# Optimization experiments

Hardware: AMD Instinct MI355X
Metric: run time of the kernel (lower is better)

## Reference

```python
import jax, jax.numpy as jnp
import numpy as np

EPS = 1e-5  # torch LayerNorm default

def ln(x, g, b):
    mu = jnp.mean(x, axis=-1, keepdims=True)
    var = jnp.mean((x - mu) ** 2, axis=-1, keepdims=True)
    return (x - mu) * jax.lax.rsqrt(var + EPS) * g + b

B, S, E, A = 131072, 199, 3, 32
D_IN = S + 1  # state_dim + 1 (time feature)

def setup_inputs() -> dict:
    key = jax.random.key(0)
    ks = iter(jax.random.split(key, 32))
    def w(shape, fan_in):
        lim = 1.0 / np.sqrt(fan_in)
        return jax.random.uniform(next(ks), shape, jnp.float32, -lim, lim)
    inp = {
        "state": jax.random.normal(next(ks), (B, S), jnp.float32),
        "time_delta": jax.random.uniform(next(ks), (B,), jnp.float32),
        # trunk: Linear(200,256)+LN, Linear(256,256)+LN, Linear(256,128)+LN
        "W1": w((D_IN, 256), D_IN), "b1": w((256,), D_IN),
        "g1": jnp.ones((256,), jnp.float32), "be1": jnp.zeros((256,), jnp.float32),
        "W2": w((256, 256), 256), "b2": w((256,), 256),
        "g2": jnp.ones((256,), jnp.float32), "be2": jnp.zeros((256,), jnp.float32),
        "W3": w((256, 128), 256), "b3": w((128,), 256),
        "g3": jnp.ones((128,), jnp.float32), "be3": jnp.zeros((128,), jnp.float32),
        # value stream
        "Wv1": w((128, 64), 128), "bv1": w((64,), 128),
        "gv": jnp.ones((64,), jnp.float32), "bev": jnp.zeros((64,), jnp.float32),
        "Wv2": w((64, 1), 64), "bv2": w((1,), 64),
        # E stacked advantage streams (all heads share action dim A)
        "Wa1": w((E, 128, 64), 128), "ba1": w((E, 64), 128),
        "ga": jnp.ones((E, 64), jnp.float32), "bea": jnp.zeros((E, 64), jnp.float32),
        "Wa2": w((E, 64, A), 64), "ba2": w((E, A), 64),
        "event_type": jax.random.randint(next(ks), (B,), 0, E),
    }
    return inp

def reference(state, time_delta,
              W1, b1, g1, be1, W2, b2, g2, be2, W3, b3, g3, be3,
              Wv1, bv1, gv, bev, Wv2, bv2,
              Wa1, ba1, ga, bea, Wa2, ba2, event_type):
    td = time_delta[:, None]                       # [B,1]
    x = jnp.concatenate([state, td], axis=1)       # [B,200]
    h = jax.nn.relu(ln(x @ W1 + b1, g1, be1))      # [B,256]
    h = jax.nn.relu(ln(h @ W2 + b2, g2, be2))      # [B,256]
    f = jax.nn.relu(ln(h @ W3 + b3, g3, be3))      # [B,128]
    v = jax.nn.relu(ln(f @ Wv1 + bv1, gv, bev)) @ Wv2 + bv2  # [B,1]
    # compute all E advantage heads, then per-sample select by event_type
    h1 = jnp.einsum('bd,edh->ebh', f, Wa1) + ba1[:, None, :]           # [E,B,64]
    h1 = jax.nn.relu(ln(h1, ga[:, None, :], bea[:, None, :]))
    adv_all = jnp.einsum('ebh,eha->eba', h1, Wa2) + ba2[:, None, :]    # [E,B,A]
    adv = jnp.take_along_axis(adv_all, event_type[None, :, None], axis=0)[0]  # [B,A]
    return v + (adv - adv.mean(axis=1, keepdims=True))
```

## Files before the change

### kernel.cpp

```cpp
#include <hip/hip_runtime.h>
#include <hip/hip_bf16.h>
#include <stdint.h>

#define DEV __device__ __forceinline__

typedef __attribute__((ext_vector_type(8))) short short8;
typedef __attribute__((ext_vector_type(4))) float floatx4;

constexpr int TM  = 64;
constexpr int NB  = 131072;
constexpr int AST = 264;

constexpr int OFF_W1 = 0;
constexpr int OFF_W2 = 57344;
constexpr int OFF_W3 = 122880;
constexpr int OFF_WH = 155648;
constexpr int OFF_WA2= 188416;
constexpr int NWQ    = 194560;

constexpr int C_B1=0, C_G1=256, C_BE1=512, C_B2=768, C_G2=1024, C_BE2=1280,
  C_B3=1536, C_G3=1664, C_BE3=1792, C_BV1=1920, C_GV=1984, C_BEV=2048,
  C_WV2=2112, C_BV2=2176, C_BA1=2177, C_GA=2369, C_BEA=2561, C_BA2=2753;
constexpr int NCONST=2849;

struct Ptrs {
  const float *state,*td,*W1,*b1,*g1,*be1,*W2,*b2,*g2,*be2,*W3,*b3,*g3,*be3,
    *Wv1,*bv1,*gv,*bev,*Wv2,*bv2,*Wa1,*ba1,*ga,*bea,*Wa2,*ba2;
  const int *et;
};

DEV unsigned short f2bf(float x){
  uint32_t u = __float_as_uint(x);
  u += 0x7fffu + ((u>>16)&1u);
  return (unsigned short)(u>>16);
}
DEV uint32_t f2bf_pk(float a, float b){
  float2 f2; f2.x=a; f2.y=b;
  __hip_bfloat162 h = __float22bfloat162_rn(f2);
  union { __hip_bfloat162 h; uint32_t u; } cv; cv.h = h;
  return cv.u;
}

__global__ void prep_kernel(Ptrs p, unsigned short* __restrict__ wq, float* __restrict__ cq){
  int idx = blockIdx.x*256 + threadIdx.x;
  if (idx < NWQ) {
    float v = 0.f;
    if (idx < OFF_W2) {
      int e = idx, w = e/14336, r = e%14336;
      int kc = r>>11, ct=(r>>9)&3, l=(r>>3)&63, j=r&7;
      int n = w*64 + ct*16 + (l&15);
      int k = kc*32 + (l>>4)*8 + j;
      if (k < 200) v = p.W1[k*256 + n];
      else if (k == 200) v = p.b1[n];
    } else if (idx < OFF_W3) {
      int e = idx-OFF_W2, w=e>>14, r=e&16383;
      int kc=r>>11, ct=(r>>9)&3, l=(r>>3)&63, j=r&7;
      int n = w*64 + ct*16 + (l&15);
      int k = kc*32 + (l>>4)*8 + j;
      int c = (k & ~63) + 16*(k&3) + ((k&63)>>2);
      v = p.W2[c*256 + n];
    } else if (idx < OFF_WH) {
      int e = idx-OFF_W3, w=e>>13, r=e&8191;
      int kc=r>>10, ct=(r>>9)&1, l=(r>>3)&63, j=r&7;
      int n = w*32 + ct*16 + (l&15);
      int k = kc*32 + (l>>4)*8 + j;
      int c = (k & ~63) + 16*(k&3) + ((k&63)>>2);
      v = p.W3[c*128 + n];
    } else if (idx < OFF_WA2) {
      int e = idx-OFF_WH, h=e>>13, r=e&8191;
      int kc=r>>11, ct=(r>>9)&3, l=(r>>3)&63, j=r&7;
      int n = ct*16 + (l&15);
      int k = kc*32 + (l>>4)*8 + j;
      int c = (k & ~31) + 16*(k&1) + ((k&31)>>1);
      v = (h<3) ? p.Wa1[h*8192 + c*64 + n] : p.Wv1[c*64 + n];
    } else {
      int e = idx-OFF_WA2, h=e>>11, r=e&2047;
      int kc=r>>10, ct=(r>>9)&1, l=(r>>3)&63, j=r&7;
      int n = ct*16 + (l&15);
      int k = kc*32 + (l>>4)*8 + j;
      int c = 16*(k&3) + (k>>2);
      v = p.Wa2[h*2048 + c*32 + n];
    }
    wq[idx] = f2bf(v);
  } else if (idx < NWQ + NCONST) {
    int ci = idx - NWQ;
    const float* src; int off;
    if      (ci < 256)  { src=p.b1;  off=ci; }
    else if (ci < 512)  { src=p.g1;  off=ci-256; }
    else if (ci < 768)  { src=p.be1; off=ci-512; }
    else if (ci < 1024) { src=p.b2;  off=ci-768; }
    else if (ci < 1280) { src=p.g2;  off=ci-1024; }
    else if (ci < 1536) { src=p.be2; off=ci-1280; }
    else if (ci < 1664) { src=p.b3;  off=ci-1536; }
    else if (ci < 1792) { src=p.g3;  off=ci-1664; }
    else if (ci < 1920) { src=p.be3; off=ci-1792; }
    else if (ci < 1984) { src=p.bv1; off=ci-1920; }
    else if (ci < 2048) { src=p.gv;  off=ci-1984; }
    else if (ci < 2112) { src=p.bev; off=ci-2048; }
    else if (ci < 2176) { src=p.Wv2; off=ci-2112; }
    else if (ci < 2177) { src=p.bv2; off=ci-2176; }
    else if (ci < 2369) { src=p.ba1; off=ci-2177; }
    else if (ci < 2561) { src=p.ga;  off=ci-2369; }
    else if (ci < 2753) { src=p.bea; off=ci-2561; }
    else                { src=p.ba2; off=ci-2753; }
    cq[ci] = src[off];
  }
}

template<int N>
DEV void loadB(short8 (&B)[N], const unsigned short* __restrict__ src, int lane){
  #pragma unroll
  for (int i=0;i<N;i++) B[i] = *(const short8*)(src + i*512 + lane*8);
}

template<int CT>
DEV void zeroAcc(floatx4 (&acc)[4][4]){
  const floatx4 z = {0.f,0.f,0.f,0.f};
  #pragma unroll
  for (int rt=0;rt<4;rt++)
    #pragma unroll
    for (int ct=0;ct<CT;ct++) acc[rt][ct]=z;
}

template<int KC,int CT>
DEV void runGemm(floatx4 (&acc)[4][4], const short8 (&B)[KC*CT],
                 const unsigned short* aBase, int aOff){
  #pragma unroll
  for (int kc=0;kc<KC;kc++){
    short8 a[4];
    #pragma unroll
    for (int rt=0;rt<4;rt++)
      a[rt] = *(const short8*)(aBase + rt*16*AST + aOff + kc*32);
    #pragma unroll
    for (int rt=0;rt<4;rt++)
      #pragma unroll
      for (int ct=0;ct<CT;ct++)
        acc[rt][ct] = __builtin_amdgcn_mfma_f32_16x16x32_bf16(a[rt], B[kc*CT+ct], acc[rt][ct], 0,0,0);
  }
}

template<int CT,bool BIAS>
DEV void statsAtomic(const floatx4 (&acc)[4][4], const float* __restrict__ cq, int bo, int colBase,
                     float* sbuf, float* ssbuf, int ln, int q, float (&bias)[4]){
  #pragma unroll
  for (int ct=0;ct<CT;ct++) bias[ct] = BIAS ? cq[bo+colBase+ct*16+ln] : 0.f;
  #pragma unroll
  for (int rt=0;rt<4;rt++){
    float s[4]={0,0,0,0}, ss[4]={0,0,0,0};
    #pragma unroll
    for (int ct=0;ct<CT;ct++){
      #pragma unroll
      for (int r=0;r<4;r++){
        float v=acc[rt][ct][r]+bias[ct];
        s[r]+=v; ss[r]+=v*v;
      }
    }
    #pragma unroll
    for (int r=0;r<4;r++){
      #pragma unroll
      for (int d=1;d<16;d<<=1){ s[r]+=__shfl_xor(s[r],d); ss[r]+=__shfl_xor(ss[r],d); }
      if (ln==0){
        int row = rt*16+q*4+r;
        atomicAdd(&sbuf[row],  s[r]);
        atomicAdd(&ssbuf[row], ss[r]);
      }
    }
  }
}

template<int CT>
DEV void lnWrite(const floatx4 (&acc)[4][4], const float* __restrict__ cq, int go, int beo, int colBase,
                 const float* sbuf, const float* ssbuf, float invN,
                 unsigned short* act_, int ln, int q, const float (&bias)[4]){
  float g[CT], be[CT];
  #pragma unroll
  for (int ct=0;ct<CT;ct++){ g[ct]=cq[go+colBase+ct*16+ln]; be[ct]=cq[beo+colBase+ct*16+ln]; }
  #pragma unroll
  for (int rt=0;rt<4;rt++){
    floatx4 sv  = *(const floatx4*)&sbuf [rt*16+q*4];
    floatx4 ssv = *(const floatx4*)&ssbuf[rt*16+q*4];
    #pragma unroll
    for (int r=0;r<4;r++){
      float mu = sv[r]*invN;
      float rs = rsqrtf(ssv[r]*invN - mu*mu + 1e-5f);
      int row=rt*16+q*4+r;
      unsigned short* pp = act_ + row*AST + colBase + ln*CT;
      float y[CT];
      #pragma unroll
      for (int ct=0;ct<CT;ct++)
        y[ct] = fmaxf((acc[rt][ct][r]+bias[ct]-mu)*rs*g[ct]+be[ct], 0.f);
      if constexpr (CT==4){
        uint2 pk; pk.x = f2bf_pk(y[0],y[1]); pk.y = f2bf_pk(y[2],y[3]);
        *(uint2*)pp = pk;
      } else {
        *(uint32_t*)pp = f2bf_pk(y[0],y[1]);
      }
    }
  }
}

__global__ __launch_bounds__(256,4) void dqn_main(
    const float* __restrict__ state, const float* __restrict__ td,
    const int* __restrict__ et, const unsigned short* __restrict__ wq,
    const float* __restrict__ cq, float* __restrict__ out)
{
  __shared__ __align__(16) unsigned short act[TM*AST];
  __shared__ float sstat[2][2][64];
  __shared__ float vbuf[64];
  __shared__ int   etl[64];

  const int tid=threadIdx.x, w=tid>>6, lane=tid&63, q=lane>>4, ln=lane&15;
  const int rowBlk = blockIdx.x*TM;

  {
    ((float*)sstat)[tid] = 0.f;
    const float* sbase = state + (size_t)rowBlk*199;
    for (int i=tid; i<64*199; i+=256){
      float v = sbase[i];
      int row = i/199, col = i - row*199;
      act[row*AST+col] = f2bf(v);
    }
    for (int i=tid; i<64*32; i+=256){
      int row = i>>5, c = 199 + (i&31);
      unsigned short hv = 0;
      if (c==199) hv = f2bf(td[rowBlk+row]);
      else if (c==200) hv = 0x3F80u;
      act[row*AST+c] = hv;
    }
    if (tid < 64) etl[tid] = et[rowBlk+tid];
  }
  __syncthreads();

  const unsigned short* aBase = act + ln*AST + q*8;
  floatx4 acc[4][4];
  float bias[4];

  {
    short8 B[28];
    loadB<28>(B, wq + OFF_W1 + w*14336, lane);
    zeroAcc<4>(acc);
    runGemm<7,4>(acc, B, aBase, 0);
  }
  statsAtomic<4,false>(acc, cq, 0, w*64, sstat[0][0], sstat[0][1], ln, q, bias);
  __syncthreads();
  lnWrite<4>(acc, cq, C_G1, C_BE1, w*64, sstat[0][0], sstat[0][1], 1.f/256.f, act, ln, q, bias);
  __syncthreads();

  {
    short8 B[32];
    loadB<32>(B, wq + OFF_W2 + w*16384, lane);
    zeroAcc<4>(acc);
    runGemm<8,4>(acc, B, aBase, 0);
  }
  statsAtomic<4,true>(acc, cq, C_B2, w*64, sstat[1][0], sstat[1][1], ln, q, bias);
  __syncthreads();
  if (tid < 128) ((float*)sstat[0])[tid] = 0.f;
  lnWrite<4>(acc, cq, C_G2, C_BE2, w*64, sstat[1][0], sstat[1][1], 1.f/256.f, act, ln, q, bias);
  __syncthreads();

  {
    short8 B[16];
    loadB<16>(B, wq + OFF_W3 + w*8192, lane);
    zeroAcc<2>(acc);
    runGemm<8,2>(acc, B, aBase, 0);
  }
  statsAtomic<2,true>(acc, cq, C_B3, w*32, sstat[0][0], sstat[0][1], ln, q, bias);
  __syncthreads();
  lnWrite<2>(acc, cq, C_G3, C_BE3, w*32, sstat[0][0], sstat[0][1], 1.f/128.f, act, ln, q, bias);
  __syncthreads();

  {
    short8 B[16];
    loadB<16>(B, wq + OFF_WH + w*8192, lane);
    zeroAcc<4>(acc);
    runGemm<4,4>(acc, B, aBase, 0);
  }
  {
    const int bo = (w<3)? C_BA1+w*64 : C_BV1;
    const int go = (w<3)? C_GA +w*64 : C_GV;
    const int beo= (w<3)? C_BEA+w*64 : C_BEV;
    float bi[4], g[4], be[4];
    #pragma unroll
    for (int ct=0;ct<4;ct++){ bi[ct]=cq[bo+ct*16+ln]; g[ct]=cq[go+ct*16+ln]; be[ct]=cq[beo+ct*16+ln]; }
    float wv[4]; float bv2v = 0.f;
    if (w==3){
      #pragma unroll
      for (int ct=0;ct<4;ct++) wv[ct]=cq[C_WV2+ct*16+ln];
      bv2v = cq[C_BV2];
    }
    #pragma unroll
    for (int rt=0;rt<4;rt++){
      float y[4][4];
      float s[4]={0,0,0,0}, ss[4]={0,0,0,0};
      #pragma unroll
      for (int ct=0;ct<4;ct++)
        #pragma unroll
        for (int r=0;r<4;r++){
          float v=acc[rt][ct][r]+bi[ct];
          y[ct][r]=v; s[r]+=v; ss[r]+=v*v;
        }
      #pragma unroll
      for (int r=0;r<4;r++){
        #pragma unroll
        for (int d=1;d<16;d<<=1){ s[r]+=__shfl_xor(s[r],d); ss[r]+=__shfl_xor(ss[r],d); }
        float mu=s[r]*(1.f/64.f);
        float rs=rsqrtf(ss[r]*(1.f/64.f)-mu*mu+1e-5f);
        #pragma unroll
        for (int ct=0;ct<4;ct++)
          y[ct][r]=fmaxf((y[ct][r]-mu)*rs*g[ct]+be[ct], 0.f);
      }

      if (w==3){
        float dd[4]={0,0,0,0};
        #pragma unroll
        for (int ct=0;ct<4;ct++)
          #pragma unroll
          for (int r=0;r<4;r++) dd[r]+=y[ct][r]*wv[ct];
        #pragma unroll
        for (int r=0;r<4;r++){
          #pragma unroll
          for (int d=1;d<16;d<<=1) dd[r]+=__shfl_xor(dd[r],d);
          if (ln==0) vbuf[rt*16+q*4+r]=dd[r]+bv2v;
        }
      } else {
        #pragma unroll
        for (int r=0;r<4;r++){
          int row=rt*16+q*4+r;
          (void)row;
        }
      }
      if (w<3){
        #pragma unroll
        for (int ct=0;ct<4;ct++)
          #pragma unroll
          for (int r=0;r<4;r++) acc[rt][ct][r]=y[ct][r];
      }
    }
  }
  __syncthreads();

  if (w<3){
    #pragma unroll
    for (int rt=0;rt<4;rt++)
      #pragma unroll
      for (int r=0;r<4;r++){
        int row=rt*16+q*4+r;
        unsigned short* pp = act + row*AST + 64*w + ln*4;
        uint2 pk;
        pk.x = f2bf_pk(acc[rt][0][r], acc[rt][1][r]);
        pk.y = f2bf_pk(acc[rt][2][r], acc[rt][3][r]);
        *(uint2*)pp = pk;
      }
    short8 B2[4];
    loadB<4>(B2, wq + OFF_WA2 + w*2048, lane);
    zeroAcc<2>(acc);
    runGemm<2,2>(acc, B2, aBase, 64*w);
    float b20 = cq[C_BA2 + w*32 + ln];
    float b21 = cq[C_BA2 + w*32 + 16 + ln];
    #pragma unroll
    for (int rt=0;rt<4;rt++)
      #pragma unroll
      for (int r=0;r<4;r++){
        float a0 = acc[rt][0][r] + b20;
        float a1 = acc[rt][1][r] + b21;
        float sm = a0 + a1;
        #pragma unroll
        for (int d=1;d<16;d<<=1) sm += __shfl_xor(sm,d);
        int row = rt*16+q*4+r;
        if (etl[row]==w){
          float vv = vbuf[row];
          float m  = sm*(1.f/32.f);
          float* op = out + (size_t)(rowBlk+row)*32 + ln;
          op[0]  = vv + a0 - m;
          op[16] = vv + a1 - m;
        }
      }
  }
}

extern "C" void kernel_launch(void* const* d_in, const int* in_sizes, int n_in,
                              void* d_out, int out_size, void* d_ws, size_t ws_size,
                              hipStream_t stream)
{
  Ptrs p;
  p.state=(const float*)d_in[0];  p.td =(const float*)d_in[1];
  p.W1 =(const float*)d_in[2];  p.b1 =(const float*)d_in[3];  p.g1 =(const float*)d_in[4];  p.be1=(const float*)d_in[5];
  p.W2 =(const float*)d_in[6];  p.b2 =(const float*)d_in[7];  p.g2 =(const float*)d_in[8];  p.be2=(const float*)d_in[9];
  p.W3 =(const float*)d_in[10]; p.b3 =(const float*)d_in[11]; p.g3 =(const float*)d_in[12]; p.be3=(const float*)d_in[13];
  p.Wv1=(const float*)d_in[14]; p.bv1=(const float*)d_in[15]; p.gv =(const float*)d_in[16]; p.bev=(const float*)d_in[17];
  p.Wv2=(const float*)d_in[18]; p.bv2=(const float*)d_in[19];
  p.Wa1=(const float*)d_in[20]; p.ba1=(const float*)d_in[21]; p.ga =(const float*)d_in[22]; p.bea=(const float*)d_in[23];
  p.Wa2=(const float*)d_in[24]; p.ba2=(const float*)d_in[25];
  p.et =(const int*)d_in[26];

  unsigned short* wq = (unsigned short*)d_ws;
  float* cq = (float*)((char*)d_ws + (size_t)NWQ*2);

  const int prepN = NWQ + NCONST;
  hipLaunchKernelGGL(prep_kernel, dim3((prepN+255)/256), dim3(256), 0, stream, p, wq, cq);
  hipLaunchKernelGGL(dqn_main, dim3(NB/TM), dim3(256), 0, stream,
                     p.state, p.td, p.et, (const unsigned short*)wq, (const float*)cq, (float*)d_out);
}
```

Baseline: 310.2 us.

## Use 128-row tiles with 512 threads and row-owned head layers per wave

```diff
diff --git a/kernel.cpp b/kernel.cpp
--- a/kernel.cpp
+++ b/kernel.cpp
@@ -7,7 +7,7 @@
 typedef __attribute__((ext_vector_type(8))) short short8;
 typedef __attribute__((ext_vector_type(4))) float floatx4;
 
-constexpr int TM  = 64;
+constexpr int TM  = 128;
 constexpr int NB  = 131072;
 constexpr int AST = 264;
 
@@ -71,7 +71,7 @@
       int kc=r>>11, ct=(r>>9)&3, l=(r>>3)&63, j=r&7;
       int n = ct*16 + (l&15);
       int k = kc*32 + (l>>4)*8 + j;
-      int c = (k & ~31) + 16*(k&1) + ((k&31)>>1);
+      int c = 16*(k&7) + (k>>3);
       v = (h<3) ? p.Wa1[h*8192 + c*64 + n] : p.Wv1[c*64 + n];
     } else {
       int e = idx-OFF_WA2, h=e>>11, r=e&2047;
@@ -107,48 +107,45 @@
   }
 }
 
-template<int N>
-DEV void loadB(short8 (&B)[N], const unsigned short* __restrict__ src, int lane){
-  #pragma unroll
-  for (int i=0;i<N;i++) B[i] = *(const short8*)(src + i*512 + lane*8);
-}
-
-template<int CT>
-DEV void zeroAcc(floatx4 (&acc)[4][4]){
+DEV void zeroAcc44(floatx4 (&acc)[4][4]){
   const floatx4 z = {0.f,0.f,0.f,0.f};
   #pragma unroll
   for (int rt=0;rt<4;rt++)
     #pragma unroll
-    for (int ct=0;ct<CT;ct++) acc[rt][ct]=z;
-}
-
-template<int KC,int CT>
-DEV void runGemm(floatx4 (&acc)[4][4], const short8 (&B)[KC*CT],
-                 const unsigned short* aBase, int aOff){
+    for (int ct=0;ct<4;ct++) acc[rt][ct]=z;
+}
+
+template<int KC>
+DEV void runGemm44(floatx4 (&acc)[4][4], const unsigned short* __restrict__ wsrc,
+                   const unsigned short* aBase, int lane){
   #pragma unroll
   for (int kc=0;kc<KC;kc++){
+    short8 b[4];
+    #pragma unroll
+    for (int ct=0;ct<4;ct++)
+      b[ct] = *(const short8*)(wsrc + kc*2048 + ct*512 + lane*8);
     short8 a[4];
     #pragma unroll
     for (int rt=0;rt<4;rt++)
-      a[rt] = *(const short8*)(aBase + rt*16*AST + aOff + kc*32);
+      a[rt] = *(const short8*)(aBase + rt*16*AST + kc*32);
     #pragma unroll
     for (int rt=0;rt<4;rt++)
       #pragma unroll
-      for (int ct=0;ct<CT;ct++)
-        acc[rt][ct] = __builtin_amdgcn_mfma_f32_16x16x32_bf16(a[rt], B[kc*CT+ct], acc[rt][ct], 0,0,0);
-  }
-}
-
-template<int CT,bool BIAS>
+      for (int ct=0;ct<4;ct++)
+        acc[rt][ct] = __builtin_amdgcn_mfma_f32_16x16x32_bf16(a[rt], b[ct], acc[rt][ct], 0,0,0);
+  }
+}
+
+template<bool BIAS>
 DEV void statsAtomic(const floatx4 (&acc)[4][4], const float* __restrict__ cq, int bo, int colBase,
-                     float* sbuf, float* ssbuf, int ln, int q, float (&bias)[4]){
-  #pragma unroll
-  for (int ct=0;ct<CT;ct++) bias[ct] = BIAS ? cq[bo+colBase+ct*16+ln] : 0.f;
+                     int rowBase, float* sbuf, float* ssbuf, int ln, int q, float (&bias)[4]){
+  #pragma unroll
+  for (int ct=0;ct<4;ct++) bias[ct] = BIAS ? cq[bo+colBase+ct*16+ln] : 0.f;
   #pragma unroll
   for (int rt=0;rt<4;rt++){
     float s[4]={0,0,0,0}, ss[4]={0,0,0,0};
     #pragma unroll
-    for (int ct=0;ct<CT;ct++){
+    for (int ct=0;ct<4;ct++){
       #pragma unroll
       for (int r=0;r<4;r++){
         float v=acc[rt][ct][r]+bias[ct];
@@ -160,7 +157,7 @@
       #pragma unroll
       for (int d=1;d<16;d<<=1){ s[r]+=__shfl_xor(s[r],d); ss[r]+=__shfl_xor(ss[r],d); }
       if (ln==0){
-        int row = rt*16+q*4+r;
+        int row = rowBase + rt*16+q*4+r;
         atomicAdd(&sbuf[row],  s[r]);
         atomicAdd(&ssbuf[row], ss[r]);
       }
@@ -168,213 +165,216 @@
   }
 }
 
-template<int CT>
-DEV void lnWrite(const floatx4 (&acc)[4][4], const float* __restrict__ cq, int go, int beo, int colBase,
-                 const float* sbuf, const float* ssbuf, float invN,
-                 unsigned short* act_, int ln, int q, const float (&bias)[4]){
-  float g[CT], be[CT];
-  #pragma unroll
-  for (int ct=0;ct<CT;ct++){ g[ct]=cq[go+colBase+ct*16+ln]; be[ct]=cq[beo+colBase+ct*16+ln]; }
+DEV void lnWrite44(const floatx4 (&acc)[4][4], const float* __restrict__ cq, int go, int beo,
+                   int colBase, int rowBase, const float* sbuf, const float* ssbuf, float invN,
+                   unsigned short* act_, int ln, int q, const float (&bias)[4]){
+  float g[4], be[4];
+  #pragma unroll
+  for (int ct=0;ct<4;ct++){ g[ct]=cq[go+colBase+ct*16+ln]; be[ct]=cq[beo+colBase+ct*16+ln]; }
   #pragma unroll
   for (int rt=0;rt<4;rt++){
-    floatx4 sv  = *(const floatx4*)&sbuf [rt*16+q*4];
-    floatx4 ssv = *(const floatx4*)&ssbuf[rt*16+q*4];
+    floatx4 sv  = *(const floatx4*)&sbuf [rowBase + rt*16+q*4];
+    floatx4 ssv = *(const floatx4*)&ssbuf[rowBase + rt*16+q*4];
     #pragma unroll
     for (int r=0;r<4;r++){
       float mu = sv[r]*invN;
       float rs = rsqrtf(ssv[r]*invN - mu*mu + 1e-5f);
-      int row=rt*16+q*4+r;
-      unsigned short* pp = act_ + row*AST + colBase + ln*CT;
-      float y[CT];
-      #pragma unroll
-      for (int ct=0;ct<CT;ct++)
+      int row = rowBase + rt*16+q*4+r;
+      float y[4];
+      #pragma unroll
+      for (int ct=0;ct<4;ct++)
         y[ct] = fmaxf((acc[rt][ct][r]+bias[ct]-mu)*rs*g[ct]+be[ct], 0.f);
-      if constexpr (CT==4){
-        uint2 pk; pk.x = f2bf_pk(y[0],y[1]); pk.y = f2bf_pk(y[2],y[3]);
-        *(uint2*)pp = pk;
-      } else {
-        *(uint32_t*)pp = f2bf_pk(y[0],y[1]);
-      }
-    }
-  }
-}
-
-__global__ __launch_bounds__(256,4) void dqn_main(
+      uint2 pk; pk.x = f2bf_pk(y[0],y[1]); pk.y = f2bf_pk(y[2],y[3]);
+      *(uint2*)(act_ + row*AST + colBase + ln*4) = pk;
+    }
+  }
+}
+
+__global__ __launch_bounds__(512,2) void dqn_main(
     const float* __restrict__ state, const float* __restrict__ td,
     const int* __restrict__ et, const unsigned short* __restrict__ wq,
     const float* __restrict__ cq, float* __restrict__ out)
 {
   __shared__ __align__(16) unsigned short act[TM*AST];
-  __shared__ float sstat[2][2][64];
-  __shared__ float vbuf[64];
-  __shared__ int   etl[64];
+  __shared__ float sstat[2][2][TM];
 
   const int tid=threadIdx.x, w=tid>>6, lane=tid&63, q=lane>>4, ln=lane&15;
+  const int wr=w>>2, wc=w&3;
   const int rowBlk = blockIdx.x*TM;
 
   {
     ((float*)sstat)[tid] = 0.f;
-    const float* sbase = state + (size_t)rowBlk*199;
-    for (int i=tid; i<64*199; i+=256){
-      float v = sbase[i];
-      int row = i/199, col = i - row*199;
-      act[row*AST+col] = f2bf(v);
-    }
-    for (int i=tid; i<64*32; i+=256){
-      int row = i>>5, c = 199 + (i&31);
-      unsigned short hv = 0;
-      if (c==199) hv = f2bf(td[rowBlk+row]);
-      else if (c==200) hv = 0x3F80u;
-      act[row*AST+c] = hv;
-    }
-    if (tid < 64) etl[tid] = et[rowBlk+tid];
+    const int row = tid>>2, t = tid&3;
+    const float* srow = state + (size_t)(rowBlk+row)*199;
+    unsigned short* arow = act + row*AST;
+    #pragma unroll
+    for (int jj=0; jj<25; jj++){
+      int c = (t*25+jj)*2;
+      float v0 = srow[c];
+      float v1 = (c==198) ? td[rowBlk+row] : srow[c+1];
+      *(uint32_t*)(arow + c) = f2bf_pk(v0, v1);
+    }
+    if (t==0) *(uint32_t*)(arow + 200) = 0x00003F80u;
+    #pragma unroll
+    for (int z=0; z<3; z++)
+      *(uint32_t*)(arow + 202 + t*6 + z*2) = 0u;
   }
   __syncthreads();
 
-  const unsigned short* aBase = act + ln*AST + q*8;
   floatx4 acc[4][4];
   float bias[4];
+  const unsigned short* aBase12 = act + (wr*64 + ln)*AST + q*8;
+
+  zeroAcc44(acc);
+  runGemm44<7>(acc, wq + OFF_W1 + wc*14336, aBase12, lane);
+  statsAtomic<false>(acc, cq, 0, wc*64, wr*64, sstat[0][0], sstat[0][1], ln, q, bias);
+  __syncthreads();
+  lnWrite44(acc, cq, C_G1, C_BE1, wc*64, wr*64, sstat[0][0], sstat[0][1], 1.f/256.f, act, ln, q, bias);
+  __syncthreads();
+
+  zeroAcc44(acc);
+  runGemm44<8>(acc, wq + OFF_W2 + wc*16384, aBase12, lane);
+  statsAtomic<true>(acc, cq, C_B2, wc*64, wr*64, sstat[1][0], sstat[1][1], ln, q, bias);
+  __syncthreads();
+  lnWrite44(acc, cq, C_G2, C_BE2, wc*64, wr*64, sstat[1][0], sstat[1][1], 1.f/256.f, act, ln, q, bias);
+  __syncthreads();
+
+  const unsigned short* aR = act + (16*w + ln)*AST + q*8;
+  int etv[4];
+  #pragma unroll
+  for (int r=0;r<4;r++) etv[r] = et[rowBlk + 16*w + q*4 + r];
 
   {
-    short8 B[28];
-    loadB<28>(B, wq + OFF_W1 + w*14336, lane);
-    zeroAcc<4>(acc);
-    runGemm<7,4>(acc, B, aBase, 0);
-  }
-  statsAtomic<4,false>(acc, cq, 0, w*64, sstat[0][0], sstat[0][1], ln, q, bias);
-  __syncthreads();
-  lnWrite<4>(acc, cq, C_G1, C_BE1, w*64, sstat[0][0], sstat[0][1], 1.f/256.f, act, ln, q, bias);
-  __syncthreads();
-
-  {
-    short8 B[32];
-    loadB<32>(B, wq + OFF_W2 + w*16384, lane);
-    zeroAcc<4>(acc);
-    runGemm<8,4>(acc, B, aBase, 0);
-  }
-  statsAtomic<4,true>(acc, cq, C_B2, w*64, sstat[1][0], sstat[1][1], ln, q, bias);
-  __syncthreads();
-  if (tid < 128) ((float*)sstat[0])[tid] = 0.f;
-  lnWrite<4>(acc, cq, C_G2, C_BE2, w*64, sstat[1][0], sstat[1][1], 1.f/256.f, act, ln, q, bias);
-  __syncthreads();
-
-  {
-    short8 B[16];
-    loadB<16>(B, wq + OFF_W3 + w*8192, lane);
-    zeroAcc<2>(acc);
-    runGemm<8,2>(acc, B, aBase, 0);
-  }
-  statsAtomic<2,true>(acc, cq, C_B3, w*32, sstat[0][0], sstat[0][1], ln, q, bias);
-  __syncthreads();
-  lnWrite<2>(acc, cq, C_G3, C_BE3, w*32, sstat[0][0], sstat[0][1], 1.f/128.f, act, ln, q, bias);
-  __syncthreads();
-
-  {
-    short8 B[16];
-    loadB<16>(B, wq + OFF_WH + w*8192, lane);
-    zeroAcc<4>(acc);
-    runGemm<4,4>(acc, B, aBase, 0);
-  }
-  {
-    const int bo = (w<3)? C_BA1+w*64 : C_BV1;
-    const int go = (w<3)? C_GA +w*64 : C_GV;
-    const int beo= (w<3)? C_BEA+w*64 : C_BEV;
+    floatx4 a8[8];
+    const floatx4 z = {0.f,0.f,0.f,0.f};
+    #pragma unroll
+    for (int nt=0;nt<8;nt++) a8[nt]=z;
+    #pragma unroll
+    for (int kc=0;kc<8;kc++){
+      short8 a = *(const short8*)(aR + kc*32);
+      #pragma unroll
+      for (int nt=0;nt<8;nt++){
+        short8 b = *(const short8*)(wq + OFF_W3 + (nt>>1)*8192 + kc*1024 + (nt&1)*512 + lane*8);
+        a8[nt] = __builtin_amdgcn_mfma_f32_16x16x32_bf16(a, b, a8[nt], 0,0,0);
+      }
+    }
+    float bi[8], g[8], be[8];
+    #pragma unroll
+    for (int nt=0;nt<8;nt++){
+      bi[nt]=cq[C_B3+nt*16+ln]; g[nt]=cq[C_G3+nt*16+ln]; be[nt]=cq[C_BE3+nt*16+ln];
+    }
+    #pragma unroll
+    for (int r=0;r<4;r++){
+      float s=0, ss=0;
+      #pragma unroll
+      for (int nt=0;nt<8;nt++){ float v=a8[nt][r]+bi[nt]; s+=v; ss+=v*v; }
+      #pragma unroll
+      for (int d=1;d<16;d<<=1){ s+=__shfl_xor(s,d); ss+=__shfl_xor(ss,d); }
+      float mu=s*(1.f/128.f), rs=rsqrtf(ss*(1.f/128.f)-mu*mu+1e-5f);
+      float y[8];
+      #pragma unroll
+      for (int nt=0;nt<8;nt++)
+        y[nt]=fmaxf((a8[nt][r]+bi[nt]-mu)*rs*g[nt]+be[nt], 0.f);
+      int row = 16*w + q*4 + r;
+      uint4 pk;
+      pk.x=f2bf_pk(y[0],y[1]); pk.y=f2bf_pk(y[2],y[3]);
+      pk.z=f2bf_pk(y[4],y[5]); pk.w=f2bf_pk(y[6],y[7]);
+      *(uint4*)(act + row*AST + ln*8) = pk;
+    }
+  }
+
+  float vrow[4];
+  float advsel[2][4] = {{0,0,0,0},{0,0,0,0}};
+  #pragma unroll
+  for (int h=0;h<4;h++){
+    int hh = (h==0)? 3 : h-1;
+    floatx4 hc[4];
+    const floatx4 z = {0.f,0.f,0.f,0.f};
+    #pragma unroll
+    for (int ct=0;ct<4;ct++) hc[ct]=z;
+    #pragma unroll
+    for (int kc=0;kc<4;kc++){
+      short8 a = *(const short8*)(aR + kc*32);
+      #pragma unroll
+      for (int ct=0;ct<4;ct++){
+        short8 b = *(const short8*)(wq + OFF_WH + hh*8192 + kc*2048 + ct*512 + lane*8);
+        hc[ct] = __builtin_amdgcn_mfma_f32_16x16x32_bf16(a, b, hc[ct], 0,0,0);
+      }
+    }
+    const int bo = (hh<3)? C_BA1+hh*64 : C_BV1;
+    const int go = (hh<3)? C_GA +hh*64 : C_GV;
+    const int beo= (hh<3)? C_BEA+hh*64 : C_BEV;
     float bi[4], g[4], be[4];
     #pragma unroll
     for (int ct=0;ct<4;ct++){ bi[ct]=cq[bo+ct*16+ln]; g[ct]=cq[go+ct*16+ln]; be[ct]=cq[beo+ct*16+ln]; }
-    float wv[4]; float bv2v = 0.f;
-    if (w==3){
+    float y[4][4];
+    #pragma unroll
+    for (int r=0;r<4;r++){
+      float s=0, ss=0;
+      #pragma unroll
+      for (int ct=0;ct<4;ct++){ float v=hc[ct][r]+bi[ct]; y[ct][r]=v; s+=v; ss+=v*v; }
+      #pragma unroll
+      for (int d=1;d<16;d<<=1){ s+=__shfl_xor(s,d); ss+=__shfl_xor(ss,d); }
+      float mu=s*(1.f/64.f), rs=rsqrtf(ss*(1.f/64.f)-mu*mu+1e-5f);
+      #pragma unroll
+      for (int ct=0;ct<4;ct++)
+        y[ct][r]=fmaxf((y[ct][r]-mu)*rs*g[ct]+be[ct], 0.f);
+    }
+    if (hh==3){
+      float wv[4];
       #pragma unroll
       for (int ct=0;ct<4;ct++) wv[ct]=cq[C_WV2+ct*16+ln];
-      bv2v = cq[C_BV2];
-    }
-    #pragma unroll
-    for (int rt=0;rt<4;rt++){
-      float y[4][4];
-      float s[4]={0,0,0,0}, ss[4]={0,0,0,0};
-      #pragma unroll
-      for (int ct=0;ct<4;ct++)
+      float bv2v = cq[C_BV2];
+      #pragma unroll
+      for (int r=0;r<4;r++){
+        float dd=0;
+        #pragma unroll
+        for (int ct=0;ct<4;ct++) dd+=y[ct][r]*wv[ct];
+        #pragma unroll
+        for (int d=1;d<16;d<<=1) dd+=__shfl_xor(dd,d);
+        vrow[r]=dd+bv2v;
+      }
+    } else {
+      #pragma unroll
+      for (int r=0;r<4;r++){
+        int row = 16*w + q*4 + r;
+        uint2 pk; pk.x=f2bf_pk(y[0][r],y[1][r]); pk.y=f2bf_pk(y[2][r],y[3][r]);
+        *(uint2*)(act + row*AST + 128 + ln*4) = pk;
+      }
+      floatx4 a2c[2];
+      const floatx4 z2 = {0.f,0.f,0.f,0.f};
+      a2c[0]=z2; a2c[1]=z2;
+      #pragma unroll
+      for (int kc=0;kc<2;kc++){
+        short8 a = *(const short8*)(act + (16*w+ln)*AST + 128 + q*8 + kc*32);
+        #pragma unroll
+        for (int ct=0;ct<2;ct++){
+          short8 b = *(const short8*)(wq + OFF_WA2 + hh*2048 + kc*1024 + ct*512 + lane*8);
+          a2c[ct] = __builtin_amdgcn_mfma_f32_16x16x32_bf16(a, b, a2c[ct], 0,0,0);
+        }
+      }
+      #pragma unroll
+      for (int ct=0;ct<2;ct++){
+        float b2v = cq[C_BA2 + hh*32 + ct*16 + ln];
         #pragma unroll
         for (int r=0;r<4;r++){
-          float v=acc[rt][ct][r]+bi[ct];
-          y[ct][r]=v; s[r]+=v; ss[r]+=v*v;
+          float av = a2c[ct][r] + b2v;
+          if (etv[r]==hh) advsel[ct][r] = av;
         }
-      #pragma unroll
-      for (int r=0;r<4;r++){
-        #pragma unroll
-        for (int d=1;d<16;d<<=1){ s[r]+=__shfl_xor(s[r],d); ss[r]+=__shfl_xor(ss[r],d); }
-        float mu=s[r]*(1.f/64.f);
-        float rs=rsqrtf(ss[r]*(1.f/64.f)-mu*mu+1e-5f);
-        #pragma unroll
-        for (int ct=0;ct<4;ct++)
-          y[ct][r]=fmaxf((y[ct][r]-mu)*rs*g[ct]+be[ct], 0.f);
-      }
-
-      if (w==3){
-        float dd[4]={0,0,0,0};
-        #pragma unroll
-        for (int ct=0;ct<4;ct++)
-          #pragma unroll
-          for (int r=0;r<4;r++) dd[r]+=y[ct][r]*wv[ct];
-        #pragma unroll
-        for (int r=0;r<4;r++){
-          #pragma unroll
-          for (int d=1;d<16;d<<=1) dd[r]+=__shfl_xor(dd[r],d);
-          if (ln==0) vbuf[rt*16+q*4+r]=dd[r]+bv2v;
-        }
-      } else {
-        #pragma unroll
-        for (int r=0;r<4;r++){
-          int row=rt*16+q*4+r;
-          (void)row;
-        }
-      }
-      if (w<3){
-        #pragma unroll
-        for (int ct=0;ct<4;ct++)
-          #pragma unroll
-          for (int r=0;r<4;r++) acc[rt][ct][r]=y[ct][r];
-      }
-    }
-  }
-  __syncthreads();
-
-  if (w<3){
-    #pragma unroll
-    for (int rt=0;rt<4;rt++)
-      #pragma unroll
-      for (int r=0;r<4;r++){
-        int row=rt*16+q*4+r;
-        unsigned short* pp = act + row*AST + 64*w + ln*4;
-        uint2 pk;
-        pk.x = f2bf_pk(acc[rt][0][r], acc[rt][1][r]);
-        pk.y = f2bf_pk(acc[rt][2][r], acc[rt][3][r]);
-        *(uint2*)pp = pk;
-      }
-    short8 B2[4];
-    loadB<4>(B2, wq + OFF_WA2 + w*2048, lane);
-    zeroAcc<2>(acc);
-    runGemm<2,2>(acc, B2, aBase, 64*w);
-    float b20 = cq[C_BA2 + w*32 + ln];
-    float b21 = cq[C_BA2 + w*32 + 16 + ln];
-    #pragma unroll
-    for (int rt=0;rt<4;rt++)
-      #pragma unroll
-      for (int r=0;r<4;r++){
-        float a0 = acc[rt][0][r] + b20;
-        float a1 = acc[rt][1][r] + b21;
-        float sm = a0 + a1;
-        #pragma unroll
-        for (int d=1;d<16;d<<=1) sm += __shfl_xor(sm,d);
-        int row = rt*16+q*4+r;
-        if (etl[row]==w){
-          float vv = vbuf[row];
-          float m  = sm*(1.f/32.f);
-          float* op = out + (size_t)(rowBlk+row)*32 + ln;
-          op[0]  = vv + a0 - m;
-          op[16] = vv + a1 - m;
-        }
-      }
+      }
+    }
+  }
+
+  #pragma unroll
+  for (int r=0;r<4;r++){
+    float sm = advsel[0][r] + advsel[1][r];
+    #pragma unroll
+    for (int d=1;d<16;d<<=1) sm += __shfl_xor(sm,d);
+    float m = sm*(1.f/32.f);
+    int row = rowBlk + 16*w + q*4 + r;
+    float* op = out + (size_t)row*32 + ln;
+    op[0]  = vrow[r] + advsel[0][r] - m;
+    op[16] = vrow[r] + advsel[1][r] - m;
   }
 }
 
@@ -398,6 +398,6 @@
 
   const int prepN = NWQ + NCONST;
   hipLaunchKernelGGL(prep_kernel, dim3((prepN+255)/256), dim3(256), 0, stream, p, wq, cq);
-  hipLaunchKernelGGL(dqn_main, dim3(NB/TM), dim3(256), 0, stream,
+  hipLaunchKernelGGL(dqn_main, dim3(NB/TM), dim3(512), 0, stream,
                      p.state, p.td, p.et, (const unsigned short*)wq, (const float*)cq, (float*)d_out);
 }
```

Result: slower. 329.7 us (+6.3%).
